# Kernel tuning notes

Measured on AMD Instinct MI355X. Metric: run time of the kernel, lower is better.

## Reference

```python
import jax, jax.numpy as jnp
import numpy as np

N_E, FEAT, REST = 2048, 512, 8
HEAD, LENGTH = 8, 64


def setup_inputs() -> dict:
    key = jax.random.key(0)
    kx, kq, kk, kd = jax.random.split(key, 4)
    x = jax.random.normal(kx, (N_E, FEAT, REST), dtype=jnp.float32)
    Q = jax.random.normal(kq, (HEAD, LENGTH, FEAT), dtype=jnp.float32)
    K = jax.random.normal(kk, (HEAD, LENGTH, FEAT), dtype=jnp.float32)
    D = jax.random.normal(kd, (HEAD, LENGTH, FEAT), dtype=jnp.float32)
    return {"x": x, "Q": Q, "K": K, "D": D}


def _linear(a, W):
    # a: (n, f, *rest), W: (h, q, f) -> y: (n, h, q, *rest)
    y = jnp.einsum('nf...,hqf->nhq...', a, W)
    # L2-normalize over the last 3 axes (here: h? no -- axes (q, rest...) per the
    # original code: sum over (-1,-2,-3) of (n,h,q,rest) = (h,q,rest) per n)
    norm = jnp.sqrt((y * y).sum((-1, -2, -3), keepdims=True))
    return y / norm


def reference(x, Q, K, D):
    n_e = x.shape[0]
    rest = x.shape[2:]
    head, length = Q.shape[0], Q.shape[1]
    q = _linear(x, Q)  # (n, h, l, rest)
    k = _linear(x, K)
    d = _linear(x, D)
    # scores over electrons: contract (l, rest) -> (h, n, n)
    w = jax.nn.softmax(jnp.einsum('nh...,mh...->hnm', q, k), axis=-1)
    # weighted combine: (h,n,m) x (m,h,l,rest) -> (n,h,l,rest)
    v = jnp.einsum('hnm,mhl...->nhl...', w, d)
    return v.reshape((n_e, head * length) + rest)
```

## Files before the change

### kernel.cpp

```cpp
#include <hip/hip_runtime.h>
#include <math.h>

#define NE   2048
#define FEAT 512

typedef short short8 __attribute__((ext_vector_type(8)));
typedef float f32x4  __attribute__((ext_vector_type(4)));

__device__ __forceinline__ unsigned short f2bf(float f) {
    union { float f; unsigned u; } v; v.f = f;
    unsigned r = v.u + 0x7fffu + ((v.u >> 16) & 1u);
    return (unsigned short)(r >> 16);
}
__device__ __forceinline__ float bf2f(unsigned b) {
    union { unsigned u; float f; } v; v.u = b << 16;
    return v.f;
}
__device__ __forceinline__ unsigned pack2(float a, float b) {
    return (unsigned)f2bf(a) | ((unsigned)f2bf(b) << 16);
}

__device__ __forceinline__ void gld16(unsigned short* lds, const unsigned short* g) {
    __builtin_amdgcn_global_load_lds(
        (const __attribute__((address_space(1))) unsigned int*)g,
        (__attribute__((address_space(3))) unsigned int*)lds,
        16, 0, 0);
}

__device__ __forceinline__ void bar() {
    asm volatile("" ::: "memory");
    __builtin_amdgcn_s_barrier();
    asm volatile("" ::: "memory");
}
#define VMW(n) asm volatile("s_waitcnt vmcnt(" #n ")" ::: "memory")


__global__ __launch_bounds__(256) void wconv_kernel(
    const float* __restrict__ Wq, const float* __restrict__ Wk, const float* __restrict__ Wd,
    unsigned short* __restrict__ wbf)
{
    const int t = threadIdx.x;
    const float* W = (blockIdx.y == 0) ? Wq : (blockIdx.y == 1) ? Wk : Wd;
    unsigned short* o = wbf + (size_t)blockIdx.y * 262144;
    const int idx = blockIdx.x * 2048 + t * 8;
    const float4* p = (const float4*)(W + idx);
    float4 v0 = p[0], v1 = p[1];
    *(uint4*)(o + idx) = make_uint4(pack2(v0.x, v0.y), pack2(v0.z, v0.w),
                                    pack2(v1.x, v1.y), pack2(v1.z, v1.w));
}

__global__ __launch_bounds__(256) void xpose_kernel(const float* __restrict__ x,
                                                    unsigned short* __restrict__ xt)
{
    __shared__ float xs[8 * 516];
    const int t = threadIdx.x;
    const int n = blockIdx.x;
    const float4* xp = (const float4*)(x + (size_t)n * 4096);
    #pragma unroll
    for (int i = 0; i < 4; ++i) {
        int idx = t + 256 * i;
        float4 v = xp[idx];
        int f = idx >> 1, rh = (idx & 1) * 4;
        xs[(rh + 0) * 516 + f] = v.x;
        xs[(rh + 1) * 516 + f] = v.y;
        xs[(rh + 2) * 516 + f] = v.z;
        xs[(rh + 3) * 516 + f] = v.w;
    }
    __syncthreads();
    const int r = t >> 5, f0 = (t & 31) * 16;
    const float* src = &xs[r * 516 + f0];
    unsigned o[8];
    #pragma unroll
    for (int j = 0; j < 8; ++j) o[j] = pack2(src[2 * j], src[2 * j + 1]);
    unsigned short* dst = xt + (size_t)n * 4096 + r * 512 + f0;
    *(uint4*)dst       = make_uint4(o[0], o[1], o[2], o[3]);
    *(uint4*)(dst + 8) = make_uint4(o[4], o[5], o[6], o[7]);
}

__global__ __launch_bounds__(512, 1) void proj_gemm(
    const unsigned short* __restrict__ wbf, const unsigned short* __restrict__ xt,
    unsigned short* __restrict__ qb, unsigned short* __restrict__ kb, unsigned short* __restrict__ db,
    float* __restrict__ s2)
{
    __shared__ unsigned short SM[49152];
    const int t = threadIdx.x;
    int bid = blockIdx.x + 128 * (blockIdx.y + 2 * blockIdx.z);
    int swz = (bid & 7) * 96 + (bid >> 3);
    const int bx = swz & 127, rest = swz >> 7;
    const int my = rest & 1, w = rest >> 1;
    const unsigned short* W = wbf + (size_t)w * 262144;
    unsigned short* out = (w == 0) ? qb : (w == 1) ? kb : db;
    const int M0 = my * 256;
    const int N0 = bx * 128;
    const int wave = t >> 6, lane = t & 63, quad = lane >> 4, l16 = lane & 15;
    const int wr = wave >> 1, wc = wave & 1;
    const int lrow = lane >> 3;
    const int scol = ((lane & 7) ^ lrow) * 8;

    f32x4 acc[4][4];
    #pragma unroll
    for (int m = 0; m < 4; ++m)
        #pragma unroll
        for (int n = 0; n < 4; ++n) acc[m][n] = {0.f, 0.f, 0.f, 0.f};

    auto STAGE = [&](int kc, int buf) {
        unsigned short* A = SM + buf * 16384;
        unsigned short* B = SM + 32768 + buf * 8192;
        #pragma unroll
        for (int p = 0; p < 4; ++p) {
            int c = p * 8 + wave;
            gld16(A + c * 512, W + (size_t)(M0 + c * 8 + lrow) * 512 + kc * 64 + scol);
        }
        #pragma unroll
        for (int p = 0; p < 2; ++p) {
            int c = p * 8 + wave;
            gld16(B + c * 512, xt + (size_t)(N0 + c * 8 + lrow) * 512 + kc * 64 + scol);
        }
    };
    auto COMPUTE = [&](int buf) {
        const unsigned short* A = SM + buf * 16384;
        const unsigned short* B = SM + 32768 + buf * 8192;
        #pragma unroll
        for (int kk = 0; kk < 2; ++kk) {
            int so = ((kk * 4 + quad) ^ (l16 & 7)) * 8;
            short8 a[4], b[4];
            #pragma unroll
            for (int m = 0; m < 4; ++m)
                a[m] = *(const short8*)&A[(wr * 64 + m * 16 + l16) * 64 + so];
            #pragma unroll
            for (int n = 0; n < 4; ++n)
                b[n] = *(const short8*)&B[(wc * 64 + n * 16 + l16) * 64 + so];
            #pragma unroll
            for (int m = 0; m < 4; ++m)
                #pragma unroll
                for (int n = 0; n < 4; ++n)
                    acc[m][n] = __builtin_amdgcn_mfma_f32_16x16x32_bf16(a[m], b[n], acc[m][n], 0, 0, 0);
        }
    };

    STAGE(0, 0);
    STAGE(1, 1);
    for (int kc = 0; kc < 8; ++kc) {
        if (kc < 7) { VMW(6); } else { VMW(0); }
        bar();
        COMPUTE(kc & 1);
        bar();
        if (kc + 2 < 8) STAGE(kc + 2, kc & 1);
    }

    float cs[4];
    #pragma unroll
    for (int n = 0; n < 4; ++n) {
        float s = 0.f;
        #pragma unroll
        for (int m = 0; m < 4; ++m)
            #pragma unroll
            for (int reg = 0; reg < 4; ++reg)
                s += acc[m][n][reg] * acc[m][n][reg];
        cs[n] = s;
    }
    #pragma unroll
    for (int n = 0; n < 4; ++n) {
        float s = cs[n];
        s += __shfl_xor(s, 16);
        s += __shfl_xor(s, 32);
        s += __shfl_xor(s, 1);
        s += __shfl_xor(s, 2);
        s += __shfl_xor(s, 4);
        if ((lane & 7) == 0 && lane < 16) {
            int n_elec = (N0 >> 3) + wc * 8 + n * 2 + (lane >> 3);
            atomicAdd(&s2[w * NE + n_elec], s);
        }
    }

    unsigned short* T = SM;
    #pragma unroll
    for (int m = 0; m < 4; ++m)
        #pragma unroll
        for (int reg = 0; reg < 4; ++reg) {
            int row = wr * 64 + m * 16 + quad * 4 + reg;
            #pragma unroll
            for (int n = 0; n < 4; ++n)
                T[row * 136 + wc * 64 + n * 16 + l16] = f2bf(acc[m][n][reg]);
        }
    __syncthreads();
    #pragma unroll
    for (int i = 0; i < 8; ++i) {
        int c = t + 512 * i;
        int row = c & 255, cb = c >> 8;
        uint4 v = *(const uint4*)(T + row * 136 + cb * 8);
        int hl = M0 + row;
        unsigned short* dst = out + (size_t)(hl >> 6) * 1048576 + (size_t)(hl & 63) * 8
                                  + (size_t)((N0 >> 3) + cb) * 512;
        *(uint4*)dst = v;
    }
}

__global__ __launch_bounds__(256) void sfinal_kernel(const float* __restrict__ s2,
                                                     float* __restrict__ scales)
{
    int i = blockIdx.x * 256 + threadIdx.x;
    scales[i] = rsqrtf(s2[i]);
}

__global__ __launch_bounds__(256) void dtrans_kernel(
    const unsigned short* __restrict__ db, const float* __restrict__ invd,
    unsigned short* __restrict__ dT)
{
    __shared__ float Ts[64 * 68];
    const int t = threadIdx.x;
    const int h = blockIdx.z, n0 = blockIdx.y * 64, f0 = blockIdx.x * 64;
    const int rr = t >> 3, cs = (t & 7) * 8;
    #pragma unroll
    for (int p = 0; p < 2; ++p) {
        int row = rr + p * 32;
        float sc = invd[n0 + row];
        uint4 v = *(const uint4*)(db + ((size_t)h * NE + n0 + row) * 512 + f0 + cs);
        unsigned a[4] = {v.x, v.y, v.z, v.w};
        float* d = &Ts[row * 68 + cs];
        #pragma unroll
        for (int j = 0; j < 4; ++j) {
            d[2 * j]     = bf2f(a[j] & 0xffffu) * sc;
            d[2 * j + 1] = bf2f(a[j] >> 16) * sc;
        }
    }
    __syncthreads();
    const int f = t >> 2, ns = (t & 3) * 16;
    unsigned o[8];
    #pragma unroll
    for (int j = 0; j < 8; ++j)
        o[j] = pack2(Ts[(ns + 2 * j) * 68 + f], Ts[(ns + 2 * j + 1) * 68 + f]);
    unsigned short* dst = dT + ((size_t)h * 512 + f0 + f) * NE + n0 + ns;
    *(uint4*)dst       = make_uint4(o[0], o[1], o[2], o[3]);
    *(uint4*)(dst + 8) = make_uint4(o[4], o[5], o[6], o[7]);
}

__global__ __launch_bounds__(512, 1) void score_kernel(
    const unsigned short* __restrict__ qb, const unsigned short* __restrict__ kb,
    const float* __restrict__ scales, unsigned short* __restrict__ P,
    float* __restrict__ sums, int g)
{
    __shared__ unsigned short SM[49152];
    const int t = threadIdx.x;
    int bid = blockIdx.x + 16 * (blockIdx.y + 8 * blockIdx.z);
    int swz = (bid & 7) * 64 + (bid >> 3);
    const int bx = swz & 15, by = (swz >> 4) & 7, bz = swz >> 7;
    const int hg = bz, h = g * 4 + hg;
    const int n0 = by * 256, m0 = bx * 128;
    const int wave = t >> 6, lane = t & 63, quad = lane >> 4, l16 = lane & 15;
    const int wr = wave >> 1, wc = wave & 1;
    const int lrow = lane >> 3;
    const int scol = ((lane & 7) ^ lrow) * 8;
    const unsigned short* qh = qb + (size_t)h * NE * 512;
    const unsigned short* kh = kb + (size_t)h * NE * 512;

    f32x4 acc[4][4];
    #pragma unroll
    for (int m = 0; m < 4; ++m)
        #pragma unroll
        for (int n = 0; n < 4; ++n) acc[m][n] = {0.f, 0.f, 0.f, 0.f};

    auto STAGE = [&](int kc, int buf) {
        unsigned short* A = SM + buf * 16384;
        unsigned short* B = SM + 32768 + buf * 8192;
        #pragma unroll
        for (int p = 0; p < 4; ++p) {
            int c = p * 8 + wave;
            gld16(A + c * 512, qh + (size_t)(n0 + c * 8 + lrow) * 512 + kc * 64 + scol);
        }
        #pragma unroll
        for (int p = 0; p < 2; ++p) {
            int c = p * 8 + wave;
            gld16(B + c * 512, kh + (size_t)(m0 + c * 8 + lrow) * 512 + kc * 64 + scol);
        }
    };
    auto COMPUTE = [&](int buf) {
        const unsigned short* A = SM + buf * 16384;
        const unsigned short* B = SM + 32768 + buf * 8192;
        #pragma unroll
        for (int kk = 0; kk < 2; ++kk) {
            int so = ((kk * 4 + quad) ^ (l16 & 7)) * 8;
            short8 a[4], b[4];
            #pragma unroll
            for (int m = 0; m < 4; ++m)
                a[m] = *(const short8*)&A[(wr * 64 + m * 16 + l16) * 64 + so];
            #pragma unroll
            for (int n = 0; n < 4; ++n)
                b[n] = *(const short8*)&B[(wc * 64 + n * 16 + l16) * 64 + so];
            #pragma unroll
            for (int m = 0; m < 4; ++m)
                #pragma unroll
                for (int n = 0; n < 4; ++n)
                    acc[m][n] = __builtin_amdgcn_mfma_f32_16x16x32_bf16(a[m], b[n], acc[m][n], 0, 0, 0);
        }
    };

    STAGE(0, 0);
    STAGE(1, 1);
    for (int kc = 0; kc < 8; ++kc) {
        if (kc < 7) { VMW(6); } else { VMW(0); }
        bar();
        COMPUTE(kc & 1);
        bar();
        if (kc + 2 < 8) STAGE(kc + 2, kc & 1);
    }

    float ik[4];
    #pragma unroll
    for (int n = 0; n < 4; ++n) ik[n] = scales[NE + m0 + wc * 64 + n * 16 + l16];

    unsigned short* T = SM;
    #pragma unroll
    for (int m = 0; m < 4; ++m)
        #pragma unroll
        for (int reg = 0; reg < 4; ++reg) {
            int row = wr * 64 + m * 16 + quad * 4 + reg;
            float qs = scales[n0 + row];
            float rs = 0.f;
            #pragma unroll
            for (int n = 0; n < 4; ++n) {
                float e = __expf(acc[m][n][reg] * qs * ik[n]);
                unsigned short bx16 = f2bf(e);
                T[row * 136 + wc * 64 + n * 16 + l16] = bx16;
                rs += bf2f(bx16);
            }
            rs += __shfl_xor(rs, 1);
            rs += __shfl_xor(rs, 2);
            rs += __shfl_xor(rs, 4);
            rs += __shfl_xor(rs, 8);
            if (l16 == 0) atomicAdd(&sums[hg * NE + n0 + row], rs);
        }
    __syncthreads();
    unsigned short* Ph = P + (size_t)hg * NE * NE;
    #pragma unroll
    for (int i = 0; i < 8; ++i) {
        int c = t + 512 * i;
        int row = c >> 4, cb = c & 15;
        uint4 v = *(const uint4*)(T + row * 136 + cb * 8);
        *(uint4*)(Ph + (size_t)(n0 + row) * NE + m0 + cb * 8) = v;
    }
}

__global__ __launch_bounds__(512) void combine_kernel(
    const unsigned short* __restrict__ P, const unsigned short* __restrict__ dT,
    const float* __restrict__ sums, float* __restrict__ out, int g)
{
    __shared__ unsigned short Ps[2][8192];
    __shared__ unsigned short Ds[2][8192];
    const int t = threadIdx.x;
    int bid = blockIdx.x + 4 * (blockIdx.y + 16 * blockIdx.z);
    int swz = (bid & 7) * 32 + (bid >> 3);
    const int bx = swz & 3, by = (swz >> 2) & 15, bz = swz >> 6;
    const int hg = bz, h = g * 4 + hg;
    const int n0 = by * 128, f0 = bx * 128;
    const int wave = t >> 6, lane = t & 63, quad = lane >> 4, l16 = lane & 15;
    const int wn = wave >> 1, wf = wave & 1;
    const int lrow = lane >> 3;
    const int scol = ((lane & 7) ^ lrow) * 8;
    const unsigned short* Ph = P + (size_t)hg * NE * NE;
    const unsigned short* dh = dT + (size_t)h * 512 * NE;

    f32x4 acc[2][4];
    #pragma unroll
    for (int i = 0; i < 2; ++i)
        #pragma unroll
        for (int j = 0; j < 4; ++j) acc[i][j] = {0.f, 0.f, 0.f, 0.f};

    auto STAGE = [&](int mc, int buf) {
        #pragma unroll
        for (int p = 0; p < 2; ++p) {
            int c = p * 8 + wave;
            gld16(&Ps[buf][c * 512], Ph + (size_t)(n0 + c * 8 + lrow) * NE + mc * 64 + scol);
            gld16(&Ds[buf][c * 512], dh + (size_t)(f0 + c * 8 + lrow) * NE + mc * 64 + scol);
        }
    };
    auto COMPUTE = [&](int buf) {
        #pragma unroll
        for (int kk = 0; kk < 2; ++kk) {
            int so = ((kk * 4 + quad) ^ (l16 & 7)) * 8;
            short8 a0 = *(const short8*)&Ps[buf][(wn * 32 + l16) * 64 + so];
            short8 a1 = *(const short8*)&Ps[buf][(wn * 32 + 16 + l16) * 64 + so];
            #pragma unroll
            for (int ct = 0; ct < 4; ++ct) {
                short8 bb = *(const short8*)&Ds[buf][(wf * 64 + ct * 16 + l16) * 64 + so];
                acc[0][ct] = __builtin_amdgcn_mfma_f32_16x16x32_bf16(a0, bb, acc[0][ct], 0, 0, 0);
                acc[1][ct] = __builtin_amdgcn_mfma_f32_16x16x32_bf16(a1, bb, acc[1][ct], 0, 0, 0);
            }
        }
    };

    STAGE(0, 0);
    STAGE(1, 1);
    for (int mc = 0; mc < 32; ++mc) {
        if (mc < 31) { VMW(4); } else { VMW(0); }
        bar();
        COMPUTE(mc & 1);
        bar();
        if (mc + 2 < 32) STAGE(mc + 2, mc & 1);
    }

    #pragma unroll
    for (int rt = 0; rt < 2; ++rt)
        #pragma unroll
        for (int reg = 0; reg < 4; ++reg) {
            int nl = wn * 32 + rt * 16 + quad * 4 + reg;
            float li = 1.0f / sums[hg * NE + n0 + nl];
            float* orow = out + (size_t)(n0 + nl) * 4096 + h * 512 + f0 + wf * 64;
            #pragma unroll
            for (int ct = 0; ct < 4; ++ct)
                orow[ct * 16 + l16] = acc[rt][ct][reg] * li;
        }
}

extern "C" void kernel_launch(void* const* d_in, const int* in_sizes, int n_in,
                              void* d_out, int out_size, void* d_ws, size_t ws_size,
                              hipStream_t stream)
{
    const float* x  = (const float*)d_in[0];
    const float* Qw = (const float*)d_in[1];
    const float* Kw = (const float*)d_in[2];
    const float* Dw = (const float*)d_in[3];
    float* out = (float*)d_out;

    char* ws = (char*)d_ws;
    unsigned short* xt = (unsigned short*)ws;
    unsigned short* db = (unsigned short*)(ws + 16777216);
    unsigned short* P  = (unsigned short*)ws;
    unsigned short* qb = (unsigned short*)(ws + 33554432);
    unsigned short* kb = (unsigned short*)(ws + 33554432 + 16777216);
    unsigned short* dT = (unsigned short*)(ws + 33554432 + 2 * 16777216);
    unsigned short* wbf = dT;
    float* scales = (float*)(ws + 83886080);
    float* sums   = (float*)(ws + 83886080 + 24576);
    float* s2     = (float*)(ws + 83886080 + 24576 + 32768);

    wconv_kernel<<<dim3(128, 3), 256, 0, stream>>>(Qw, Kw, Dw, wbf);
    xpose_kernel<<<2048, 256, 0, stream>>>(x, xt);
    hipMemsetAsync(s2, 0, 3 * NE * sizeof(float), stream);
    proj_gemm<<<dim3(128, 2, 3), 512, 0, stream>>>(wbf, xt, qb, kb, db, s2);
    sfinal_kernel<<<24, 256, 0, stream>>>(s2, scales);
    dtrans_kernel<<<dim3(8, 32, 8), 256, 0, stream>>>(db, scales + 2 * NE, dT);
    for (int g = 0; g < 2; ++g) {
        hipMemsetAsync(sums, 0, 4 * NE * sizeof(float), stream);
        score_kernel<<<dim3(16, 8, 4), 512, 0, stream>>>(qb, kb, scales, P, sums, g);
        combine_kernel<<<dim3(4, 16, 4), 512, 0, stream>>>(P, dT, sums, out, g);
    }
}
```

Baseline: 271.7 us.

## Fold rsqrt into consumers and double combine K-chunk to 128

Result: no change. 268.4 us (-1.2%).

```diff
diff --git a/kernel.cpp b/kernel.cpp
--- a/kernel.cpp
+++ b/kernel.cpp
@@ -196,15 +196,8 @@
     }
 }
 
-__global__ __launch_bounds__(256) void sfinal_kernel(const float* __restrict__ s2,
-                                                     float* __restrict__ scales)
-{
-    int i = blockIdx.x * 256 + threadIdx.x;
-    scales[i] = rsqrtf(s2[i]);
-}
-
 __global__ __launch_bounds__(256) void dtrans_kernel(
-    const unsigned short* __restrict__ db, const float* __restrict__ invd,
+    const unsigned short* __restrict__ db, const float* __restrict__ s2d,
     unsigned short* __restrict__ dT)
 {
     __shared__ float Ts[64 * 68];
@@ -214,7 +207,7 @@
     #pragma unroll
     for (int p = 0; p < 2; ++p) {
         int row = rr + p * 32;
-        float sc = invd[n0 + row];
+        float sc = rsqrtf(s2d[n0 + row]);
         uint4 v = *(const uint4*)(db + ((size_t)h * NE + n0 + row) * 512 + f0 + cs);
         unsigned a[4] = {v.x, v.y, v.z, v.w};
         float* d = &Ts[row * 68 + cs];
@@ -237,7 +230,7 @@
 
 __global__ __launch_bounds__(512, 1) void score_kernel(
     const unsigned short* __restrict__ qb, const unsigned short* __restrict__ kb,
-    const float* __restrict__ scales, unsigned short* __restrict__ P,
+    const float* __restrict__ s2, unsigned short* __restrict__ P,
     float* __restrict__ sums, int g)
 {
     __shared__ unsigned short SM[49152];
@@ -307,7 +300,7 @@
 
     float ik[4];
     #pragma unroll
-    for (int n = 0; n < 4; ++n) ik[n] = scales[NE + m0 + wc * 64 + n * 16 + l16];
+    for (int n = 0; n < 4; ++n) ik[n] = rsqrtf(s2[NE + m0 + wc * 64 + n * 16 + l16]);
 
     unsigned short* T = SM;
     #pragma unroll
@@ -315,7 +308,7 @@
         #pragma unroll
         for (int reg = 0; reg < 4; ++reg) {
             int row = wr * 64 + m * 16 + quad * 4 + reg;
-            float qs = scales[n0 + row];
+            float qs = rsqrtf(s2[n0 + row]);
             float rs = 0.f;
             #pragma unroll
             for (int n = 0; n < 4; ++n) {
@@ -341,12 +334,12 @@
     }
 }
 
-__global__ __launch_bounds__(512) void combine_kernel(
+__global__ __launch_bounds__(512, 1) void combine_kernel(
     const unsigned short* __restrict__ P, const unsigned short* __restrict__ dT,
     const float* __restrict__ sums, float* __restrict__ out, int g)
 {
-    __shared__ unsigned short Ps[2][8192];
-    __shared__ unsigned short Ds[2][8192];
+    __shared__ unsigned short Ps[2][16384];
+    __shared__ unsigned short Ds[2][16384];
     const int t = threadIdx.x;
     int bid = blockIdx.x + 4 * (blockIdx.y + 16 * blockIdx.z);
     int swz = (bid & 7) * 32 + (bid >> 3);
@@ -355,8 +348,7 @@
     const int n0 = by * 128, f0 = bx * 128;
     const int wave = t >> 6, lane = t & 63, quad = lane >> 4, l16 = lane & 15;
     const int wn = wave >> 1, wf = wave & 1;
-    const int lrow = lane >> 3;
-    const int scol = ((lane & 7) ^ lrow) * 8;
+    const int lrow4 = lane >> 4;
     const unsigned short* Ph = P + (size_t)hg * NE * NE;
     const unsigned short* dh = dT + (size_t)h * 512 * NE;
 
@@ -368,21 +360,29 @@
 
     auto STAGE = [&](int mc, int buf) {
         #pragma unroll
-        for (int p = 0; p < 2; ++p) {
-            int c = p * 8 + wave;
-            gld16(&Ps[buf][c * 512], Ph + (size_t)(n0 + c * 8 + lrow) * NE + mc * 64 + scol);
-            gld16(&Ds[buf][c * 512], dh + (size_t)(f0 + c * 8 + lrow) * NE + mc * 64 + scol);
+        for (int p = 0; p < 4; ++p) {
+            int c = p * 8 + wave;
+            int row = c * 4 + lrow4;
+            int sb = ((lane & 15) ^ (row & 15)) * 8;
+            gld16(&Ps[buf][c * 512], Ph + (size_t)(n0 + row) * NE + mc * 128 + sb);
+        }
+        #pragma unroll
+        for (int p = 0; p < 4; ++p) {
+            int c = p * 8 + wave;
+            int row = c * 4 + lrow4;
+            int sb = ((lane & 15) ^ (row & 15)) * 8;
+            gld16(&Ds[buf][c * 512], dh + (size_t)(f0 + row) * NE + mc * 128 + sb);
         }
     };
     auto COMPUTE = [&](int buf) {
         #pragma unroll
-        for (int kk = 0; kk < 2; ++kk) {
-            int so = ((kk * 4 + quad) ^ (l16 & 7)) * 8;
-            short8 a0 = *(const short8*)&Ps[buf][(wn * 32 + l16) * 64 + so];
-            short8 a1 = *(const short8*)&Ps[buf][(wn * 32 + 16 + l16) * 64 + so];
+        for (int kk = 0; kk < 4; ++kk) {
+            int so = ((kk * 4 + quad) ^ l16) * 8;
+            short8 a0 = *(const short8*)&Ps[buf][(wn * 32 + l16) * 128 + so];
+            short8 a1 = *(const short8*)&Ps[buf][(wn * 32 + 16 + l16) * 128 + so];
             #pragma unroll
             for (int ct = 0; ct < 4; ++ct) {
-                short8 bb = *(const short8*)&Ds[buf][(wf * 64 + ct * 16 + l16) * 64 + so];
+                short8 bb = *(const short8*)&Ds[buf][(wf * 64 + ct * 16 + l16) * 128 + so];
                 acc[0][ct] = __builtin_amdgcn_mfma_f32_16x16x32_bf16(a0, bb, acc[0][ct], 0, 0, 0);
                 acc[1][ct] = __builtin_amdgcn_mfma_f32_16x16x32_bf16(a1, bb, acc[1][ct], 0, 0, 0);
             }
@@ -391,12 +391,12 @@
 
     STAGE(0, 0);
     STAGE(1, 1);
-    for (int mc = 0; mc < 32; ++mc) {
-        if (mc < 31) { VMW(4); } else { VMW(0); }
+    for (int mc = 0; mc < 16; ++mc) {
+        if (mc < 15) { VMW(8); } else { VMW(0); }
         bar();
         COMPUTE(mc & 1);
         bar();
-        if (mc + 2 < 32) STAGE(mc + 2, mc & 1);
+        if (mc + 2 < 16) STAGE(mc + 2, mc & 1);
     }
 
     #pragma unroll
@@ -430,19 +430,17 @@
     unsigned short* kb = (unsigned short*)(ws + 33554432 + 16777216);
     unsigned short* dT = (unsigned short*)(ws + 33554432 + 2 * 16777216);
     unsigned short* wbf = dT;
-    float* scales = (float*)(ws + 83886080);
-    float* sums   = (float*)(ws + 83886080 + 24576);
-    float* s2     = (float*)(ws + 83886080 + 24576 + 32768);
+    float* sums   = (float*)(ws + 83886080);
+    float* s2     = (float*)(ws + 83886080 + 32768);
 
     wconv_kernel<<<dim3(128, 3), 256, 0, stream>>>(Qw, Kw, Dw, wbf);
     xpose_kernel<<<2048, 256, 0, stream>>>(x, xt);
     hipMemsetAsync(s2, 0, 3 * NE * sizeof(float), stream);
     proj_gemm<<<dim3(128, 2, 3), 512, 0, stream>>>(wbf, xt, qb, kb, db, s2);
-    sfinal_kernel<<<24, 256, 0, stream>>>(s2, scales);
-    dtrans_kernel<<<dim3(8, 32, 8), 256, 0, stream>>>(db, scales + 2 * NE, dT);
+    dtrans_kernel<<<dim3(8, 32, 8), 256, 0, stream>>>(db, s2 + 2 * NE, dT);
     for (int g = 0; g < 2; ++g) {
         hipMemsetAsync(sums, 0, 4 * NE * sizeof(float), stream);
-        score_kernel<<<dim3(16, 8, 4), 512, 0, stream>>>(qb, kb, scales, P, sums, g);
+        score_kernel<<<dim3(16, 8, 4), 512, 0, stream>>>(qb, kb, s2, P, sums, g);
         combine_kernel<<<dim3(4, 16, 4), 512, 0, stream>>>(P, dT, sums, out, g);
     }
 }
```
